# Kernel optimization log

Hardware: AMD Instinct MI355X
Metric: run time of the kernel (lower is better)

Reference implementation:

```python
import jax, jax.numpy as jnp
import numpy as np

H, DK = 8, 64  # n_head, d_k (= d_v)
LN_EPS = 1e-6


def _layer_norm(x, g, b):
    mu = jnp.mean(x, axis=-1, keepdims=True)
    var = jnp.var(x, axis=-1, keepdims=True)
    return (x - mu) * jax.lax.rsqrt(var + LN_EPS) * g + b


def setup_inputs() -> dict:
    key = jax.random.key(0)
    ks = jax.random.split(key, 8)
    B, S, D, DF = 8, 1024, 512, 2048
    s = 0.02
    return {
        "enc_input": jax.random.normal(ks[0], (B, S, D), jnp.float32),
        "cost_mat": jax.random.normal(ks[1], (B, S, S), jnp.float32),
        "wq": jax.random.normal(ks[2], (D, D), jnp.float32) * s,
        "wk": jax.random.normal(ks[3], (D, D), jnp.float32) * s,
        "wv": jax.random.normal(ks[4], (D, D), jnp.float32) * s,
        "fc_w": jax.random.normal(ks[5], (D, D), jnp.float32) * s,
        "ln1_g": jnp.ones((D,), jnp.float32),
        "ln1_b": jnp.zeros((D,), jnp.float32),
        "w1": jax.random.normal(ks[6], (DF, D), jnp.float32) * s,
        "b1": jnp.zeros((DF,), jnp.float32),
        "w2": jax.random.normal(ks[7], (D, DF), jnp.float32) * s,
        "b2": jnp.zeros((D,), jnp.float32),
        "ln2_g": jnp.ones((D,), jnp.float32),
        "ln2_b": jnp.zeros((D,), jnp.float32),
    }


def reference(enc_input, cost_mat, wq, wk, wv, fc_w, ln1_g, ln1_b,
              w1, b1, w2, b2, ln2_g, ln2_b):
    B, S, D = enc_input.shape
    # Q/K/V projections -> [B, H, S, dk]
    q = (enc_input @ wq.T).reshape(B, S, H, DK).transpose(0, 2, 1, 3)
    k = (enc_input @ wk.T).reshape(B, S, H, DK).transpose(0, 2, 1, 3)
    v = (enc_input @ wv.T).reshape(B, S, H, DK).transpose(0, 2, 1, 3)
    # mixed score: scaled QK^T plus cost matrix broadcast over heads
    scores = jnp.einsum("bhqd,bhkd->bhqk", q, k) / np.sqrt(DK).astype(np.float32)
    scores = scores + cost_mat[:, None, :, :]
    attn = jax.nn.softmax(scores, axis=-1)
    ctx = jnp.einsum("bhqk,bhkd->bhqd", attn, v)  # [B,H,S,dk]
    ctx = ctx.transpose(0, 2, 1, 3).reshape(B, S, D)
    attn_out = _layer_norm(ctx @ fc_w.T + enc_input, ln1_g, ln1_b)
    # position-wise FFN with residual + layernorm
    h = jax.nn.relu(attn_out @ w1.T + b1)
    ffn = h @ w2.T + b2
    return _layer_norm(ffn + attn_out, ln2_g, ln2_b)
```

## Files before the change

kernel.cpp:

```cpp
#include <hip/hip_runtime.h>
#include <stdint.h>

typedef __attribute__((ext_vector_type(8))) short bf16x8;
typedef __attribute__((ext_vector_type(4))) float f32x4;

__device__ __forceinline__ unsigned short f2bf(float f) {
  unsigned int u = __builtin_bit_cast(unsigned int, f);
  u += 0x7fffu + ((u >> 16) & 1u);
  return (unsigned short)(u >> 16);
}

__device__ __forceinline__ float bf2f(unsigned short u) {
  unsigned int x = ((unsigned int)u) << 16;
  return __builtin_bit_cast(float, x);
}

__device__ __forceinline__ void gload16(const void* g, void* l) {
  __builtin_amdgcn_global_load_lds(
      (const __attribute__((address_space(1))) void*)g,
      (__attribute__((address_space(3))) void*)l, 16, 0, 0);
}

__global__ void cvt_all(const float* __restrict__ enc,
                        const float* __restrict__ cost,
                        const float* __restrict__ wq,
                        const float* __restrict__ wk,
                        const float* __restrict__ wv,
                        const float* __restrict__ fcw,
                        const float* __restrict__ w1,
                        const float* __restrict__ w2,
                        unsigned short* __restrict__ enc_bf,
                        unsigned short* __restrict__ cost_bf,
                        unsigned short* __restrict__ wqkv_bf,
                        unsigned short* __restrict__ fcw_bf,
                        unsigned short* __restrict__ w1_bf,
                        unsigned short* __restrict__ w2_bf) {
  const int i = blockIdx.x * 256 + threadIdx.x;
  constexpr int E0 = 1048576;
  constexpr int E1 = E0 + 2097152;
  constexpr int E2 = E1 + 65536;
  constexpr int E3 = E2 + 65536;
  constexpr int E4 = E3 + 65536;
  constexpr int E5 = E4 + 65536;
  constexpr int E6 = E5 + 262144;
  constexpr int E7 = E6 + 262144;
  const float* in;
  unsigned short* out;
  int base;
  float scale = 1.0f;
  if (i < E0)      { in = enc;  out = enc_bf;            base = 0;  }
  else if (i < E1) { in = cost; out = cost_bf;           base = E0; scale = 1.44269504f; }
  else if (i < E2) { in = wq;   out = wqkv_bf;           base = E1; }
  else if (i < E3) { in = wk;   out = wqkv_bf + 262144;  base = E2; }
  else if (i < E4) { in = wv;   out = wqkv_bf + 524288;  base = E3; }
  else if (i < E5) { in = fcw;  out = fcw_bf;            base = E4; }
  else if (i < E6) { in = w1;   out = w1_bf;             base = E5; }
  else if (i < E7) { in = w2;   out = w2_bf;             base = E6; }
  else return;
  const int k = i - base;
  float4 v = ((const float4*)in)[k];
  ushort4 o;
  o.x = f2bf(v.x * scale);
  o.y = f2bf(v.y * scale);
  o.z = f2bf(v.z * scale);
  o.w = f2bf(v.w * scale);
  ((ushort4*)out)[k] = o;
}

template <int EPI>
__global__ __launch_bounds__(256, 2) void gemm_bt(
    const unsigned short* __restrict__ A, const unsigned short* __restrict__ B,
    void* __restrict__ C, const float* __restrict__ bias, int M, int N, int K) {
  __shared__ unsigned short Al[2][128 * 32];
  __shared__ unsigned short Bl[2][128 * 32];
  const int tid = threadIdx.x;
  const int lane = tid & 63;
  const int wid = tid >> 6;
  const int wr = wid >> 1;
  const int wc = wid & 1;
  const int m0 = blockIdx.y * 128;
  const int n0 = blockIdx.x * 128;

  f32x4 acc[4][4];
#pragma unroll
  for (int i = 0; i < 4; ++i)
#pragma unroll
    for (int j = 0; j < 4; ++j) acc[i][j] = f32x4{0.f, 0.f, 0.f, 0.f};

  const int srow = wid * 32 + (lane >> 2);
  const int scol = (lane & 3) * 8;
  const unsigned short* Ag = A + (size_t)(m0 + srow) * K + scol;
  const unsigned short* Bg = B + (size_t)(n0 + srow) * K + scol;
  const size_t K16 = (size_t)16 * K;

  auto stage = [&](int buf, int kt) {
    unsigned short* Ald = &Al[buf][wid * 1024];
    unsigned short* Bld = &Bl[buf][wid * 1024];
    gload16(Ag + kt, Ald);
    gload16(Ag + K16 + kt, Ald + 512);
    gload16(Bg + kt, Bld);
    gload16(Bg + K16 + kt, Bld + 512);
  };

  const int ko = (lane >> 4) * 8;
  const int arow = wr * 64 + (lane & 15);
  const int brow = wc * 64 + (lane & 15);

  stage(0, 0);
  __syncthreads();
  for (int kt = 0, it = 0; kt < K; kt += 32, ++it) {
    const int cur = it & 1;
    if (kt + 32 < K) stage(cur ^ 1, kt + 32);
    bf16x8 af[4], bf[4];
#pragma unroll
    for (int mi = 0; mi < 4; ++mi)
      af[mi] = *(const bf16x8*)&Al[cur][(arow + mi * 16) * 32 + ko];
#pragma unroll
    for (int ni = 0; ni < 4; ++ni)
      bf[ni] = *(const bf16x8*)&Bl[cur][(brow + ni * 16) * 32 + ko];
#pragma unroll
    for (int mi = 0; mi < 4; ++mi)
#pragma unroll
      for (int ni = 0; ni < 4; ++ni)
        acc[mi][ni] = __builtin_amdgcn_mfma_f32_16x16x32_bf16(
            af[mi], bf[ni], acc[mi][ni], 0, 0, 0);
    __syncthreads();
  }

  const int rl = (lane >> 4) * 4;
  const int cl = lane & 15;
#pragma unroll
  for (int mi = 0; mi < 4; ++mi) {
#pragma unroll
    for (int ni = 0; ni < 4; ++ni) {
      const int r0 = m0 + wr * 64 + mi * 16 + rl;
      const int c = n0 + wc * 64 + ni * 16 + cl;
      if (EPI == 5 && c >= 1024) {
        unsigned short* Vt = (unsigned short*)C + (size_t)2 * 8192 * 512;
        const int cc = c - 1024;
        ushort4 pk;
        pk.x = f2bf(acc[mi][ni][0]);
        pk.y = f2bf(acc[mi][ni][1]);
        pk.z = f2bf(acc[mi][ni][2]);
        pk.w = f2bf(acc[mi][ni][3]);
        const int b_ = r0 >> 10, s_ = r0 & 1023, h_ = cc >> 6, dd = cc & 63;
        *(ushort4*)(Vt + ((size_t)((b_ * 8 + h_) * 64 + dd) * 1024 + s_)) = pk;
      } else if (EPI == 5) {
        unsigned short* dst =
            (c < 512) ? (unsigned short*)C + (size_t)r0 * 512 + c
                      : (unsigned short*)C + (size_t)8192 * 512 +
                            (size_t)r0 * 512 + (c - 512);
#pragma unroll
        for (int j = 0; j < 4; ++j) dst[(size_t)j * 512] = f2bf(acc[mi][ni][j]);
      } else {
#pragma unroll
        for (int j = 0; j < 4; ++j) {
          float v = acc[mi][ni][j];
          if (EPI == 2 || EPI == 6) v += bias[c];
          if (EPI == 2) v = fmaxf(v, 0.f);
          ((unsigned short*)C)[(size_t)(r0 + j) * N + c] = f2bf(v);
        }
      }
    }
  }
}

template <int EPI>
__global__ __launch_bounds__(256, 2) void gemm_bt64(
    const unsigned short* __restrict__ A, const unsigned short* __restrict__ B,
    void* __restrict__ C, const float* __restrict__ bias, int M, int N, int K) {
  __shared__ unsigned short Al[2][64 * 32];
  __shared__ unsigned short Bl[2][128 * 32];
  const int tid = threadIdx.x;
  const int lane = tid & 63;
  const int wid = tid >> 6;
  const int m0 = blockIdx.y * 64;
  const int n0 = blockIdx.x * 128;

  f32x4 acc[4][2];
#pragma unroll
  for (int i = 0; i < 4; ++i)
#pragma unroll
    for (int j = 0; j < 2; ++j) acc[i][j] = f32x4{0.f, 0.f, 0.f, 0.f};

  const int srow = tid >> 2;
  const int scol = (tid & 3) * 8;
  const unsigned short* Ag = A + (size_t)(m0 + srow) * K + scol;
  const unsigned short* Bg = B + (size_t)(n0 + srow) * K + scol;
  const size_t K64 = (size_t)64 * K;

  auto stage = [&](int buf, int kt) {
    gload16(Ag + kt, &Al[buf][wid * 512]);
    gload16(Bg + kt, &Bl[buf][wid * 512]);
    gload16(Bg + K64 + kt, &Bl[buf][2048 + wid * 512]);
  };

  const int ko = (lane >> 4) * 8;
  const int cl16 = lane & 15;

  stage(0, 0);
  __syncthreads();
  for (int kt = 0, it = 0; kt < K; kt += 32, ++it) {
    const int cur = it & 1;
    if (kt + 32 < K) stage(cur ^ 1, kt + 32);
    bf16x8 af[4], bf[2];
#pragma unroll
    for (int mi = 0; mi < 4; ++mi)
      af[mi] = *(const bf16x8*)&Al[cur][(mi * 16 + cl16) * 32 + ko];
#pragma unroll
    for (int ni = 0; ni < 2; ++ni)
      bf[ni] = *(const bf16x8*)&Bl[cur][(wid * 32 + ni * 16 + cl16) * 32 + ko];
#pragma unroll
    for (int mi = 0; mi < 4; ++mi)
#pragma unroll
      for (int ni = 0; ni < 2; ++ni)
        acc[mi][ni] = __builtin_amdgcn_mfma_f32_16x16x32_bf16(
            af[mi], bf[ni], acc[mi][ni], 0, 0, 0);
    __syncthreads();
  }

  const int rl = (lane >> 4) * 4;
#pragma unroll
  for (int mi = 0; mi < 4; ++mi) {
#pragma unroll
    for (int ni = 0; ni < 2; ++ni) {
      const int r0 = m0 + mi * 16 + rl;
      const int c = n0 + wid * 32 + ni * 16 + cl16;
#pragma unroll
      for (int j = 0; j < 4; ++j) {
        float v = acc[mi][ni][j];
        if (EPI == 6) v += bias[c];
        ((unsigned short*)C)[(size_t)(r0 + j) * N + c] = f2bf(v);
      }
    }
  }
}

__global__ __launch_bounds__(512, 4) void attn_kernel(
    const unsigned short* __restrict__ Q, const unsigned short* __restrict__ K,
    const unsigned short* __restrict__ V,
    const unsigned short* __restrict__ Cb,
    unsigned short* __restrict__ ctx) {
  __shared__ unsigned short Kl[2][4096];
  __shared__ unsigned short Vl[2][4096];
  __shared__ unsigned short Cl[8192];
  __shared__ unsigned short P[8][1024];
  const int tid = threadIdx.x, lane = tid & 63, wid = tid >> 6;
  const int bh = blockIdx.y, b = bh >> 3, h = bh & 7;
  const int q0 = blockIdx.x * 128;
  const int qw = q0 + wid * 16;
  const int cl = lane & 15, gl = lane >> 4;

  const unsigned short* qp =
      Q + (size_t)(b * 1024 + qw + cl) * 512 + h * 64 + gl * 8;
  const bf16x8 qf0 = *(const bf16x8*)qp;
  const bf16x8 qf1 = *(const bf16x8*)(qp + 32);

  f32x4 acc[4];
  float lsum = 0.f;
#pragma unroll
  for (int i = 0; i < 4; ++i) acc[i] = f32x4{0.f, 0.f, 0.f, 0.f};

  const int srow = tid >> 3;
  const int swzc = ((tid & 7) * 8) ^ ((srow & 7) << 3);
  const unsigned short* Ksrc =
      K + (size_t)(b * 1024 + srow) * 512 + h * 64 + swzc;
  const unsigned short* Vsrc = V + (size_t)(bh * 64 + srow) * 1024 + swzc;
  const unsigned short* Csrc =
      Cb + (size_t)(b * 1024 + q0 + srow) * 1024 + swzc;

  auto stage_kv = [&](int buf, int k0) {
    gload16(Ksrc + (size_t)k0 * 512, &Kl[buf][wid * 512]);
    gload16(Vsrc + k0, &Vl[buf][wid * 512]);
  };
  auto stage_c = [&](int k0) {
    gload16(Csrc + k0, &Cl[wid * 512]);
    gload16(Csrc + (size_t)64 * 1024 + k0, &Cl[4096 + wid * 512]);
  };

  const int ks = (cl & 7) << 3;
  const int pswz = (cl & 7) << 3;
  const int crow = wid * 16 + cl;

  stage_kv(0, 0);
  stage_c(0);
  __syncthreads();

  for (int t = 0; t < 16; ++t) {
    const int cur = t & 1;
    if (t < 15) stage_kv(cur ^ 1, (t + 1) * 64);

#pragma unroll
    for (int ni = 0; ni < 4; ++ni) {
      const int krow = ni * 16 + cl;
      bf16x8 k0f = *(const bf16x8*)&Kl[cur][krow * 64 + ((gl * 8) ^ ks)];
      bf16x8 k1f = *(const bf16x8*)&Kl[cur][krow * 64 + ((32 + gl * 8) ^ ks)];
      f32x4 t2 = f32x4{0.f, 0.f, 0.f, 0.f};
      t2 = __builtin_amdgcn_mfma_f32_16x16x32_bf16(k0f, qf0, t2, 0, 0, 0);
      t2 = __builtin_amdgcn_mfma_f32_16x16x32_bf16(k1f, qf1, t2, 0, 0, 0);
      const uint2 cpk = *(const uint2*)&Cl[crow * 64 + ((ni * 16 + gl * 4) ^ pswz)];
      float p0, p1, p2, p3;
      {
        float e0 = __builtin_fmaf(t2[0], 0.18033688f, bf2f((unsigned short)(cpk.x & 0xffff)));
        float e1 = __builtin_fmaf(t2[1], 0.18033688f, bf2f((unsigned short)(cpk.x >> 16)));
        float e2 = __builtin_fmaf(t2[2], 0.18033688f, bf2f((unsigned short)(cpk.y & 0xffff)));
        float e3 = __builtin_fmaf(t2[3], 0.18033688f, bf2f((unsigned short)(cpk.y >> 16)));
        asm("v_exp_f32 %0, %1" : "=v"(p0) : "v"(e0));
        asm("v_exp_f32 %0, %1" : "=v"(p1) : "v"(e1));
        asm("v_exp_f32 %0, %1" : "=v"(p2) : "v"(e2));
        asm("v_exp_f32 %0, %1" : "=v"(p3) : "v"(e3));
      }
      lsum += (p0 + p1) + (p2 + p3);
      uint32_t lo, hi;
      asm("v_cvt_pk_bf16_f32 %0, %1, %2" : "=v"(lo) : "v"(p0), "v"(p1));
      asm("v_cvt_pk_bf16_f32 %0, %1, %2" : "=v"(hi) : "v"(p2), "v"(p3));
      *(uint2*)&P[wid][cl * 64 + ((ni * 16 + gl * 4) ^ pswz)] = uint2{lo, hi};
    }
    __builtin_amdgcn_sched_barrier(0);
    __builtin_amdgcn_s_barrier();
    __builtin_amdgcn_sched_barrier(0);
    if (t < 15) stage_c((t + 1) * 64);

    bf16x8 pf0 = *(const bf16x8*)&P[wid][cl * 64 + ((gl * 8) ^ pswz)];
    bf16x8 pf1 = *(const bf16x8*)&P[wid][cl * 64 + ((32 + gl * 8) ^ pswz)];
#pragma unroll
    for (int nv = 0; nv < 4; ++nv) {
      const int vrow = nv * 16 + cl;
      bf16x8 v0f = *(const bf16x8*)&Vl[cur][vrow * 64 + ((gl * 8) ^ ks)];
      bf16x8 v1f = *(const bf16x8*)&Vl[cur][vrow * 64 + ((32 + gl * 8) ^ ks)];
      acc[nv] =
          __builtin_amdgcn_mfma_f32_16x16x32_bf16(pf0, v0f, acc[nv], 0, 0, 0);
      acc[nv] =
          __builtin_amdgcn_mfma_f32_16x16x32_bf16(pf1, v1f, acc[nv], 0, 0, 0);
    }
    __syncthreads();
  }

  lsum += __shfl_xor(lsum, 16);
  lsum += __shfl_xor(lsum, 32);
  const float linv = 1.0f / lsum;
  float linvw[4];
#pragma unroll
  for (int j = 0; j < 4; ++j) linvw[j] = __shfl(linv, gl * 4 + j);
#pragma unroll
  for (int nv = 0; nv < 4; ++nv)
#pragma unroll
    for (int j = 0; j < 4; ++j) {
      float v = acc[nv][j] * linvw[j];
      ctx[(size_t)(b * 1024 + qw + gl * 4 + j) * 512 + h * 64 + nv * 16 + cl] =
          f2bf(v);
    }
}

template <int OUT_F32>
__global__ __launch_bounds__(256) void ln_kernel(
    const unsigned short* __restrict__ x1, const unsigned short* __restrict__ x2,
    const float* __restrict__ g, const float* __restrict__ bt,
    void* __restrict__ out) {
  const int lane = threadIdx.x & 63, wid = threadIdx.x >> 6;
  const int row = blockIdx.x * 4 + wid;
  const bf16x8 a = *(const bf16x8*)(x1 + (size_t)row * 512 + lane * 8);
  const bf16x8 bb = *(const bf16x8*)(x2 + (size_t)row * 512 + lane * 8);
  float x[8];
#pragma unroll
  for (int i = 0; i < 8; ++i)
    x[i] = bf2f((unsigned short)a[i]) + bf2f((unsigned short)bb[i]);
  float sum = 0.f, sq = 0.f;
#pragma unroll
  for (int i = 0; i < 8; ++i) {
    sum += x[i];
    sq += x[i] * x[i];
  }
#pragma unroll
  for (int m = 1; m <= 32; m <<= 1) {
    sum += __shfl_xor(sum, m);
    sq += __shfl_xor(sq, m);
  }
  const float mean = sum * (1.f / 512.f);
  const float var = sq * (1.f / 512.f) - mean * mean;
  const float rstd = rsqrtf(var + 1e-6f);
  float y[8];
#pragma unroll
  for (int i = 0; i < 8; ++i) {
    const int c = lane * 8 + i;
    y[i] = (x[i] - mean) * rstd * g[c] + bt[c];
  }
  if (OUT_F32) {
    float4* op = (float4*)((float*)out + (size_t)row * 512);
    op[lane * 2] = make_float4(y[0], y[1], y[2], y[3]);
    op[lane * 2 + 1] = make_float4(y[4], y[5], y[6], y[7]);
  } else {
    bf16x8 o;
#pragma unroll
    for (int i = 0; i < 8; ++i) o[i] = (short)f2bf(y[i]);
    *(bf16x8*)((unsigned short*)out + (size_t)row * 512 + lane * 8) = o;
  }
}

extern "C" void kernel_launch(void* const* d_in, const int* in_sizes, int n_in,
                              void* d_out, int out_size, void* d_ws,
                              size_t ws_size, hipStream_t stream) {
  const float* enc = (const float*)d_in[0];
  const float* cost = (const float*)d_in[1];
  const float* wq = (const float*)d_in[2];
  const float* wk = (const float*)d_in[3];
  const float* wv = (const float*)d_in[4];
  const float* fcw = (const float*)d_in[5];
  const float* ln1g = (const float*)d_in[6];
  const float* ln1b = (const float*)d_in[7];
  const float* w1 = (const float*)d_in[8];
  const float* b1 = (const float*)d_in[9];
  const float* w2 = (const float*)d_in[10];
  const float* b2 = (const float*)d_in[11];
  const float* ln2g = (const float*)d_in[12];
  const float* ln2b = (const float*)d_in[13];

  char* ws = (char*)d_ws;
  size_t off = 0;
  auto alloc = [&](size_t n) {
    void* p = ws + off;
    off += (n + 255) & ~(size_t)255;
    return p;
  };
  const size_t MD = 8192ull * 512;
  const size_t MF = 8192ull * 2048;
  unsigned short* enc_bf = (unsigned short*)alloc(MD * 2);
  unsigned short* wqkv_bf = (unsigned short*)alloc(3 * 512 * 512 * 2);
  unsigned short* fcw_bf = (unsigned short*)alloc(512 * 512 * 2);
  unsigned short* w1_bf = (unsigned short*)alloc(2048 * 512 * 2);
  unsigned short* w2_bf = (unsigned short*)alloc(512 * 2048 * 2);
  unsigned short* Qb = (unsigned short*)alloc(MD * 2 * 3);
  unsigned short* Kb = Qb + MD;
  unsigned short* Vt = Kb + MD;
  unsigned short* ctx_bf = (unsigned short*)alloc(MD * 2);
  unsigned short* fc_bf = (unsigned short*)alloc(MD * 2);
  unsigned short* attn_bf = (unsigned short*)alloc(MD * 2);
  unsigned short* ffn_bf = (unsigned short*)alloc(MD * 2);
  unsigned short* h_bf = (unsigned short*)alloc(MF * 2);
  unsigned short* cost_bf = h_bf;

  cvt_all<<<15360, 256, 0, stream>>>(enc, cost, wq, wk, wv, fcw, w1, w2,
                                     enc_bf, cost_bf, wqkv_bf, fcw_bf, w1_bf,
                                     w2_bf);

  gemm_bt<5><<<dim3(12, 64), 256, 0, stream>>>(enc_bf, wqkv_bf, Qb, nullptr,
                                               8192, 1536, 512);
  attn_kernel<<<dim3(8, 64), 512, 0, stream>>>(Qb, Kb, Vt, cost_bf, ctx_bf);
  gemm_bt64<0><<<dim3(4, 128), 256, 0, stream>>>(ctx_bf, fcw_bf, fc_bf,
                                                 nullptr, 8192, 512, 512);
  ln_kernel<0><<<2048, 256, 0, stream>>>(fc_bf, enc_bf, ln1g, ln1b, attn_bf);
  gemm_bt<2><<<dim3(16, 64), 256, 0, stream>>>(attn_bf, w1_bf, h_bf, b1, 8192,
                                               2048, 512);
  gemm_bt64<6><<<dim3(4, 128), 256, 0, stream>>>(h_bf, w2_bf, ffn_bf, b2, 8192,
                                                 512, 2048);
  ln_kernel<1><<<2048, 256, 0, stream>>>(ffn_bf, attn_bf, ln2g, ln2b, d_out);
}
```

Measured before the change: 159.6 us.

## Split-K the N=512 GEMMs into two partials reduced inside layernorm

The fc and FFN-down GEMMs (N=512) now run with a grid z-dimension of 2, each block computing half of K and writing its own bf16 partial buffer. The layernorm kernels read both partials plus the residual and add the bias, which removes the bias epilogue from the GEMM. The aim is to double the block count (512 to 1024) so the device is better filled and the long K=2048 loop is halved. The cost is extra partial-buffer writes and reads, plus an extra bf16 rounding of each partial.

```diff
diff --git a/kernel.cpp b/kernel.cpp
--- a/kernel.cpp
+++ b/kernel.cpp
@@ -156,8 +156,7 @@
 #pragma unroll
         for (int j = 0; j < 4; ++j) {
           float v = acc[mi][ni][j];
-          if (EPI == 2 || EPI == 6) v += bias[c];
-          if (EPI == 2) v = fmaxf(v, 0.f);
+          if (EPI == 2) v = fmaxf(v + bias[c], 0.f);
           ((unsigned short*)C)[(size_t)(r0 + j) * N + c] = f2bf(v);
         }
       }
@@ -165,10 +164,10 @@
   }
 }
 
-template <int EPI>
 __global__ __launch_bounds__(256, 2) void gemm_bt64(
     const unsigned short* __restrict__ A, const unsigned short* __restrict__ B,
-    void* __restrict__ C, const float* __restrict__ bias, int M, int N, int K) {
+    unsigned short* __restrict__ C0, unsigned short* __restrict__ C1,
+    int M, int N, int Khalf, int Kstride) {
   __shared__ unsigned short Al[2][64 * 32];
   __shared__ unsigned short Bl[2][128 * 32];
   const int tid = threadIdx.x;
@@ -176,6 +175,10 @@
   const int wid = tid >> 6;
   const int m0 = blockIdx.y * 64;
   const int n0 = blockIdx.x * 128;
+  const int kz = blockIdx.z;
+  const unsigned short* Ab = A + (size_t)kz * Khalf;
+  const unsigned short* Bb = B + (size_t)kz * Khalf;
+  unsigned short* C = kz ? C1 : C0;
 
   f32x4 acc[4][2];
 #pragma unroll
@@ -185,9 +188,9 @@
 
   const int srow = tid >> 2;
   const int scol = (tid & 3) * 8;
-  const unsigned short* Ag = A + (size_t)(m0 + srow) * K + scol;
-  const unsigned short* Bg = B + (size_t)(n0 + srow) * K + scol;
-  const size_t K64 = (size_t)64 * K;
+  const unsigned short* Ag = Ab + (size_t)(m0 + srow) * Kstride + scol;
+  const unsigned short* Bg = Bb + (size_t)(n0 + srow) * Kstride + scol;
+  const size_t K64 = (size_t)64 * Kstride;
 
   auto stage = [&](int buf, int kt) {
     gload16(Ag + kt, &Al[buf][wid * 512]);
@@ -200,9 +203,9 @@
 
   stage(0, 0);
   __syncthreads();
-  for (int kt = 0, it = 0; kt < K; kt += 32, ++it) {
+  for (int kt = 0, it = 0; kt < Khalf; kt += 32, ++it) {
     const int cur = it & 1;
-    if (kt + 32 < K) stage(cur ^ 1, kt + 32);
+    if (kt + 32 < Khalf) stage(cur ^ 1, kt + 32);
     bf16x8 af[4], bf[2];
 #pragma unroll
     for (int mi = 0; mi < 4; ++mi)
@@ -227,11 +230,8 @@
       const int r0 = m0 + mi * 16 + rl;
       const int c = n0 + wid * 32 + ni * 16 + cl16;
 #pragma unroll
-      for (int j = 0; j < 4; ++j) {
-        float v = acc[mi][ni][j];
-        if (EPI == 6) v += bias[c];
-        ((unsigned short*)C)[(size_t)(r0 + j) * N + c] = f2bf(v);
-      }
+      for (int j = 0; j < 4; ++j)
+        C[(size_t)(r0 + j) * N + c] = f2bf(acc[mi][ni][j]);
     }
   }
 }
@@ -354,17 +354,25 @@
 
 template <int OUT_F32>
 __global__ __launch_bounds__(256) void ln_kernel(
-    const unsigned short* __restrict__ x1, const unsigned short* __restrict__ x2,
+    const unsigned short* __restrict__ x1a,
+    const unsigned short* __restrict__ x1b,
+    const unsigned short* __restrict__ x2, const float* __restrict__ bias,
     const float* __restrict__ g, const float* __restrict__ bt,
     void* __restrict__ out) {
   const int lane = threadIdx.x & 63, wid = threadIdx.x >> 6;
   const int row = blockIdx.x * 4 + wid;
-  const bf16x8 a = *(const bf16x8*)(x1 + (size_t)row * 512 + lane * 8);
+  const bf16x8 a = *(const bf16x8*)(x1a + (size_t)row * 512 + lane * 8);
+  const bf16x8 a2 = *(const bf16x8*)(x1b + (size_t)row * 512 + lane * 8);
   const bf16x8 bb = *(const bf16x8*)(x2 + (size_t)row * 512 + lane * 8);
   float x[8];
 #pragma unroll
   for (int i = 0; i < 8; ++i)
-    x[i] = bf2f((unsigned short)a[i]) + bf2f((unsigned short)bb[i]);
+    x[i] = bf2f((unsigned short)a[i]) + bf2f((unsigned short)a2[i]) +
+           bf2f((unsigned short)bb[i]);
+  if (bias) {
+#pragma unroll
+    for (int i = 0; i < 8; ++i) x[i] += bias[lane * 8 + i];
+  }
   float sum = 0.f, sq = 0.f;
 #pragma unroll
   for (int i = 0; i < 8; ++i) {
@@ -433,9 +441,11 @@
   unsigned short* Kb = Qb + MD;
   unsigned short* Vt = Kb + MD;
   unsigned short* ctx_bf = (unsigned short*)alloc(MD * 2);
-  unsigned short* fc_bf = (unsigned short*)alloc(MD * 2);
+  unsigned short* fc_p0 = (unsigned short*)alloc(MD * 2);
+  unsigned short* fc_p1 = (unsigned short*)alloc(MD * 2);
   unsigned short* attn_bf = (unsigned short*)alloc(MD * 2);
-  unsigned short* ffn_bf = (unsigned short*)alloc(MD * 2);
+  unsigned short* ffn_p0 = (unsigned short*)alloc(MD * 2);
+  unsigned short* ffn_p1 = (unsigned short*)alloc(MD * 2);
   unsigned short* h_bf = (unsigned short*)alloc(MF * 2);
   unsigned short* cost_bf = h_bf;
 
@@ -446,12 +456,14 @@
   gemm_bt<5><<<dim3(12, 64), 256, 0, stream>>>(enc_bf, wqkv_bf, Qb, nullptr,
                                                8192, 1536, 512);
   attn_kernel<<<dim3(8, 64), 512, 0, stream>>>(Qb, Kb, Vt, cost_bf, ctx_bf);
-  gemm_bt64<0><<<dim3(4, 128), 256, 0, stream>>>(ctx_bf, fcw_bf, fc_bf,
-                                                 nullptr, 8192, 512, 512);
-  ln_kernel<0><<<2048, 256, 0, stream>>>(fc_bf, enc_bf, ln1g, ln1b, attn_bf);
+  gemm_bt64<<<dim3(4, 128, 2), 256, 0, stream>>>(ctx_bf, fcw_bf, fc_p0, fc_p1,
+                                                 8192, 512, 256, 512);
+  ln_kernel<0><<<2048, 256, 0, stream>>>(fc_p0, fc_p1, enc_bf, nullptr, ln1g,
+                                         ln1b, attn_bf);
   gemm_bt<2><<<dim3(16, 64), 256, 0, stream>>>(attn_bf, w1_bf, h_bf, b1, 8192,
                                                2048, 512);
-  gemm_bt64<6><<<dim3(4, 128), 256, 0, stream>>>(h_bf, w2_bf, ffn_bf, b2, 8192,
-                                                 512, 2048);
-  ln_kernel<1><<<2048, 256, 0, stream>>>(ffn_bf, attn_bf, ln2g, ln2b, d_out);
-}
+  gemm_bt64<<<dim3(4, 128, 2), 256, 0, stream>>>(h_bf, w2_bf, ffn_p0, ffn_p1,
+                                                 8192, 512, 1024, 2048);
+  ln_kernel<1><<<2048, 256, 0, stream>>>(ffn_p0, ffn_p1, attn_bf, b2, ln2g,
+                                         ln2b, d_out);
+}
```

After: 174.6 us. +9.4%, slower.
